# Performance work log

Measured on AMD Instinct MI355X. Metric: run time of the kernel, lower is better.

The kernel has to match this reference:

```python
import jax, jax.numpy as jnp
import numpy as np

N_NODES = 325
C = 64
BATCH = 64
SEQ = 12
K = 3


def setup_inputs() -> dict:
    key = jax.random.key(0)
    k1, k2, k3 = jax.random.split(key, 3)
    x = jax.random.normal(k1, (BATCH, C, N_NODES, SEQ), dtype=jnp.float32)
    # sparse-ish binary adjacency with self loops (typical traffic graph density)
    a = (jax.random.uniform(k2, (N_NODES, N_NODES)) < 0.05).astype(jnp.float32)
    adj = jnp.maximum(a, a.T)
    adj = adj.at[jnp.arange(N_NODES), jnp.arange(N_NODES)].set(1.0)
    W = jax.random.normal(k3, (K, C, C), dtype=jnp.float32) * (1.0 / np.sqrt(C))
    b = jnp.zeros((C,), dtype=jnp.float32)
    return {"x": x, "adj": adj, "W": W, "b": b}


def reference(x, adj, W, b):
    B, c_in, N, T = x.shape
    # [B, C, N, T] -> [B*T, N, C]
    xr = jnp.transpose(x, (0, 3, 2, 1)).reshape(-1, N, c_in)
    # symmetric normalized Laplacian L = I - D^{-1/2} A D^{-1/2}
    d = adj.sum(axis=-1)
    d_inv_sqrt = jnp.where(d > 0, jax.lax.rsqrt(d), 0.0)
    norm_adj = d_inv_sqrt[:, None] * adj * d_inv_sqrt[None, :]
    L = jnp.eye(N, dtype=adj.dtype) - norm_adj
    # Chebyshev recursion, K=3
    Tx0 = xr
    Tx1 = jnp.einsum('ij,bjc->bic', L, Tx0)
    out = jnp.einsum('bnc,cd->bnd', Tx0, W[0]) + jnp.einsum('bnc,cd->bnd', Tx1, W[1])
    Tx2 = 2.0 * jnp.einsum('ij,bjc->bic', L, Tx1) - Tx0
    out = out + jnp.einsum('bnc,cd->bnd', Tx2, W[2]) + b
    # [B*T, N, C] -> [B, C, N, T]
    out = out.reshape(B, T, N, c_in)
    return jnp.transpose(out, (0, 3, 2, 1))
```

## Files before the change

kernel.cpp:

```cpp
#include <hip/hip_runtime.h>
#include <hip/hip_bf16.h>

#define NND   325
#define SEQ   12
#define NT    3900
#define KP    352
#define NC    11
#define CHUNK_SHORTS 12288
#define MROWS 48
#define NTILE 22

typedef __attribute__((ext_vector_type(8))) short short8;
typedef __attribute__((ext_vector_type(4))) float floatx4;

static __device__ __forceinline__ unsigned short f2bf(float f) {
    unsigned int u = __float_as_uint(f);
    unsigned int r = (u + 0x7fffu + ((u >> 16) & 1u)) >> 16;
    return (unsigned short)r;
}

static __device__ __forceinline__ int xi(int m, int j) {
    int slot = (j >> 3) ^ ((m >> 1) & 3);
    return m * KP + slot * 8 + (j & 7);
}
static __device__ __forceinline__ int swz(int n) {
    return ((n & 7) ^ ((n >> 3) & 7)) << 4;
}

__global__ void calc_dis(const float* __restrict__ adj, float* __restrict__ dis) {
    int i = blockIdx.x;
    const float* row = adj + (size_t)i * NND;
    float s = 0.f;
    for (int j = threadIdx.x; j < NND; j += 64) s += row[j];
    for (int o = 32; o; o >>= 1) s += __shfl_down(s, o);
    if (threadIdx.x == 0) dis[i] = (s > 0.f) ? rsqrtf(s) : 0.f;
}

__global__ void build_L2(const float* __restrict__ adj, const float* __restrict__ dis,
                         unsigned short* __restrict__ Lg2) {
    int s = blockIdx.x * 256 + threadIdx.x;
    if (s >= NC * CHUNK_SHORTS) return;
    int c = s / CHUNK_SHORTS, r = s - c * CHUNK_SHORTS;
    int n = r >> 5, w = r & 31;
    int j = c * 32 + w;
    float v = 0.f;
    if (n < NND && j < NND) {
        float a = adj[(size_t)n * NND + j];
        v = ((n == j) ? 1.f : 0.f) - dis[n] * a * dis[j];
    }
    Lg2[s] = f2bf(v);
}

__global__ void build_wswz(const float* __restrict__ W, unsigned short* __restrict__ wswz) {
    int idx = blockIdx.x * 256 + threadIdx.x;
    if (idx >= 64 * 192) return;
    int d = idx / 192, k = idx - d * 192;
    int kind = k >> 6, c = k & 63;
    float wv = W[kind * 4096 + c * 64 + d];
    float w;
    if (kind == 0)      w = wv - W[2 * 4096 + c * 64 + d];
    else if (kind == 1) w = wv;
    else                w = 2.f * wv;
    int byte = d * 384 + ((2 * k) ^ swz(d));
    wswz[byte >> 1] = f2bf(w);
}

__global__ __launch_bounds__(512, 4) void cheb_mfma(
        const float* __restrict__ x,
        const unsigned short* __restrict__ Lg2,
        unsigned short* __restrict__ Yg,
        unsigned short* __restrict__ Zg) {
    __shared__ __align__(16) unsigned short Xs[MROWS * KP];
    __shared__ __align__(16) unsigned short Ys[MROWS * KP];

    const int tid = threadIdx.x;
    int bid = blockIdx.x;
    bid = (bid & 7) * 128 + (bid >> 3);
    const int g0 = bid * 4;

    const int w  = tid >> 6;
    const int l  = tid & 63;
    const int lm = l & 15, lg = l >> 4;
    const int ap = (lm >> 1) & 3;

    const unsigned short* lp[3];
    #pragma unroll
    for (int i = 0; i < 3; ++i) {
        int ti = w * 3 + i;
        int nrow = ti * 16 + lm;
        lp[i] = Lg2 + (size_t)nrow * 32 + lg * 8;
    }
    const int nown = (w * 3 + 2 < NTILE) ? 3 : (NTILE - w * 3 < 0 ? 0 : NTILE - w * 3);

    for (int i = tid; i < MROWS * 27; i += 512) {
        int m = i / 27, j = 325 + (i - (i / 27) * 27);
        Xs[xi(m, j)] = 0;
    }
    const float4* xb = (const float4*)(x + (size_t)g0 * NT);
    for (int i = tid; i < 3900; i += 512) {
        float4 v = xb[i];
        int f = i * 4;
        int gl = f / NT;
        int rem = f - gl * NT;
        int j = rem / SEQ;
        int t0 = rem - j * SEQ;
        int m = gl * SEQ + t0;
        Xs[xi(m + 0, j)] = f2bf(v.x);
        Xs[xi(m + 1, j)] = f2bf(v.y);
        Xs[xi(m + 2, j)] = f2bf(v.z);
        Xs[xi(m + 3, j)] = f2bf(v.w);
    }
    __syncthreads();

    floatx4 acc[3][3];

    auto zero_acc = [&]() {
        #pragma unroll
        for (int a = 0; a < 3; ++a)
            #pragma unroll
            for (int b2 = 0; b2 < 3; ++b2) acc[a][b2] = (floatx4){0.f, 0.f, 0.f, 0.f};
    };

    auto gemm = [&](const unsigned short* Aimg) {
        #pragma unroll
        for (int c = 0; c < NC; ++c) {
            short8 bf[3];
            #pragma unroll
            for (int i = 0; i < 3; ++i)
                if (i < nown)
                    bf[i] = *(const short8*)(lp[i] + (size_t)c * CHUNK_SHORTS);
            short8 af[3];
            #pragma unroll
            for (int mt = 0; mt < 3; ++mt) {
                int m = mt * 16 + lm;
                int slot = (c * 4 + lg) ^ ap;
                af[mt] = *(const short8*)&Aimg[m * KP + slot * 8];
            }
            #pragma unroll
            for (int i = 0; i < 3; ++i)
                if (i < nown)
                    #pragma unroll
                    for (int mt = 0; mt < 3; ++mt)
                        acc[mt][i] = __builtin_amdgcn_mfma_f32_16x16x32_bf16(
                            af[mt], bf[i], acc[mt][i], 0, 0, 0);
        }
    };

    auto store_acc = [&](unsigned short* img) {
        #pragma unroll
        for (int i = 0; i < 3; ++i) {
            if (i < nown) {
                int n = (w * 3 + i) * 16 + lm;
                #pragma unroll
                for (int mt = 0; mt < 3; ++mt)
                    #pragma unroll
                    for (int r = 0; r < 4; ++r)
                        img[xi(mt * 16 + lg * 4 + r, n)] = f2bf(acc[mt][i][r]);
            }
        }
    };

    auto copy_out = [&](const unsigned short* img, unsigned short* dst) {
        for (int i = tid; i < 1950 * 2; i += 512) {
            int gl = i / 975;
            int r2 = i - gl * 975;
            int n = r2 / 3;
            int tq = (r2 - n * 3) * 4;
            int m = gl * SEQ + tq;
            ushort4 u;
            u.x = img[xi(m + 0, n)];
            u.y = img[xi(m + 1, n)];
            u.z = img[xi(m + 2, n)];
            u.w = img[xi(m + 3, n)];
            *(ushort4*)&dst[(size_t)(g0 + gl) * NT + n * SEQ + tq] = u;
        }
    };

    zero_acc();
    gemm(Xs);
    store_acc(Ys);
    __syncthreads();
    copy_out(Ys, Yg);

    zero_acc();
    gemm(Ys);
    store_acc(Xs);
    __syncthreads();
    copy_out(Xs, Zg);
}

__global__ __launch_bounds__(256) void mix_mfma(
        const float* __restrict__ x,
        const unsigned short* __restrict__ Yg,
        const unsigned short* __restrict__ Zg,
        const unsigned short* __restrict__ wswz,
        const float* __restrict__ bias,
        float* __restrict__ out) {
    __shared__ unsigned short Bl[96 * 192];
    __shared__ unsigned short Al[64 * 192];
    const int tid = threadIdx.x;
    int lin = blockIdx.x;
    lin = (lin & 7) * 328 + (lin >> 3);
    const int b = lin / 41;
    const int nt0 = (lin - b * 41) * 96;
    const bool tail = (nt0 + 96 > NT);

    for (int i = tid; i < 1536; i += 256)
        *(short8*)((char*)Al + i * 16) = *(const short8*)((const char*)wswz + i * 16);

    for (int i = tid; i < 768; i += 256) {
        int r = i / 12, ch = i - r * 12;
        int nt = nt0 + ch * 8;
        const float* sp = x + ((size_t)b * 64 + r) * NT + nt;
        float f[8];
        if (!tail || nt + 8 <= NT) {
            float4 v0 = *(const float4*)sp;
            float4 v1 = *(const float4*)(sp + 4);
            f[0] = v0.x; f[1] = v0.y; f[2] = v0.z; f[3] = v0.w;
            f[4] = v1.x; f[5] = v1.y; f[6] = v1.z; f[7] = v1.w;
        } else {
            #pragma unroll
            for (int jj = 0; jj < 8; ++jj) f[jj] = (nt + jj < NT) ? sp[jj] : 0.f;
        }
        int k2 = 2 * r;
        #pragma unroll
        for (int jj = 0; jj < 8; ++jj) {
            int n = ch * 8 + jj;
            *(unsigned short*)((char*)Bl + n * 384 + (k2 ^ swz(n))) = f2bf(f[jj]);
        }
    }
    for (int i = tid; i < 1536; i += 256) {
        int r = 64 + i / 12, ch = i % 12;
        int nt = nt0 + ch * 8;
        const unsigned short* base = (r < 128) ? Yg : Zg;
        const unsigned short* sp = base + ((size_t)b * 64 + (r & 63)) * NT + nt;
        unsigned short f[8];
        if (!tail || nt + 8 <= NT) {
            ushort4 v0 = *(const ushort4*)sp;
            ushort4 v1 = *(const ushort4*)(sp + 4);
            f[0] = v0.x; f[1] = v0.y; f[2] = v0.z; f[3] = v0.w;
            f[4] = v1.x; f[5] = v1.y; f[6] = v1.z; f[7] = v1.w;
        } else {
            #pragma unroll
            for (int jj = 0; jj < 8; ++jj) f[jj] = (nt + jj < NT) ? sp[jj] : (unsigned short)0;
        }
        int k2 = 2 * r;
        #pragma unroll
        for (int jj = 0; jj < 8; ++jj) {
            int n = ch * 8 + jj;
            *(unsigned short*)((char*)Bl + n * 384 + (k2 ^ swz(n))) = f[jj];
        }
    }
    __syncthreads();

    const int w = __builtin_amdgcn_readfirstlane(tid >> 6);
    const int l = tid & 63;
    const int lm = l & 15, lg = l >> 4;

    floatx4 acc[6];
    #pragma unroll
    for (int i = 0; i < 6; ++i) acc[i] = (floatx4){0.f, 0.f, 0.f, 0.f};

    const int arow = w * 16 + lm;
    const char* Ab = (const char*)Al + arow * 384;
    #pragma unroll
    for (int ks = 0; ks < 6; ++ks) {
        const int k2 = (ks * 32 + lg * 8) * 2;
        short8 a = *(const short8*)(Ab + (k2 ^ swz(arow)));
        #pragma unroll
        for (int ni = 0; ni < 6; ++ni) {
            int n = ni * 16 + lm;
            short8 bb = *(const short8*)((const char*)Bl + n * 384 + (k2 ^ swz(n)));
            acc[ni] = __builtin_amdgcn_mfma_f32_16x16x32_bf16(a, bb, acc[ni], 0, 0, 0);
        }
    }

    float br[4];
    #pragma unroll
    for (int j = 0; j < 4; ++j) br[j] = bias[w * 16 + lg * 4 + j];
    #pragma unroll
    for (int ni = 0; ni < 6; ++ni) {
        int nt = nt0 + ni * 16 + lm;
        if (nt < NT) {
            float* op = out + ((size_t)b * 64 + w * 16 + lg * 4) * NT + nt;
            #pragma unroll
            for (int j = 0; j < 4; ++j) op[(size_t)j * NT] = acc[ni][j] + br[j];
        }
    }
}

extern "C" void kernel_launch(void* const* d_in, const int* in_sizes, int n_in,
                              void* d_out, int out_size, void* d_ws, size_t ws_size,
                              hipStream_t stream) {
    const float* x   = (const float*)d_in[0];
    const float* adj = (const float*)d_in[1];
    const float* W   = (const float*)d_in[2];
    const float* b   = (const float*)d_in[3];
    float* out = (float*)d_out;

    char* ws = (char*)d_ws;
    float* dis           = (float*)(ws + 0);
    unsigned short* Lg2  = (unsigned short*)(ws + 1312);
    unsigned short* wswz = (unsigned short*)(ws + 271648);
    unsigned short* Yg   = (unsigned short*)(ws + 296224);
    unsigned short* Zg   = (unsigned short*)(ws + 32245024);

    calc_dis<<<NND, 64, 0, stream>>>(adj, dis);
    build_L2<<<(NC * CHUNK_SHORTS + 255) / 256, 256, 0, stream>>>(adj, dis, Lg2);
    build_wswz<<<48, 256, 0, stream>>>(W, wswz);
    cheb_mfma<<<1024, 512, 0, stream>>>(x, Lg2, Yg, Zg);
    mix_mfma<<<2624, 256, 0, stream>>>(x, Yg, Zg, wswz, b, out);
}
```

Measured before the change: 125.6 us.

## Store Chebyshev intermediates in time-major padded layout with vectorized LDS/global stores

Swaps the MFMA operand roles so each lane's accumulator holds four consecutive nodes for one time row, which allows ushort4 stores into the swizzled LDS image. The global Y/Z intermediates now use a [group][t][node] layout padded to 328 nodes per row, so copy_out moves 16-byte vectors straight from LDS. The mix kernel then gathers a node range per time step with this stride, with no tail handling. This cuts the scalar LDS traffic and the narrow global stores, at the cost of a strided re-gather in the mix kernel and reads of padded node columns.

```diff
diff --git a/kernel.cpp b/kernel.cpp
--- a/kernel.cpp
+++ b/kernel.cpp
@@ -9,6 +9,8 @@
 #define CHUNK_SHORTS 12288
 #define MROWS 48
 #define NTILE 22
+#define TROW  328
+#define GROW  3936
 
 typedef __attribute__((ext_vector_type(8))) short short8;
 typedef __attribute__((ext_vector_type(4))) float floatx4;
@@ -86,8 +88,7 @@
     const unsigned short* lp[3];
     #pragma unroll
     for (int i = 0; i < 3; ++i) {
-        int ti = w * 3 + i;
-        int nrow = ti * 16 + lm;
+        int nrow = (w * 3 + i) * 16 + lm;
         lp[i] = Lg2 + (size_t)nrow * 32 + lg * 8;
     }
     const int nown = (w * 3 + 2 < NTILE) ? 3 : (NTILE - w * 3 < 0 ? 0 : NTILE - w * 3);
@@ -121,28 +122,28 @@
             for (int b2 = 0; b2 < 3; ++b2) acc[a][b2] = (floatx4){0.f, 0.f, 0.f, 0.f};
     };
 
-    auto gemm = [&](const unsigned short* Aimg) {
+    auto gemm = [&](const unsigned short* Bimg) {
         #pragma unroll
         for (int c = 0; c < NC; ++c) {
-            short8 bf[3];
+            short8 lf[3];
             #pragma unroll
             for (int i = 0; i < 3; ++i)
                 if (i < nown)
-                    bf[i] = *(const short8*)(lp[i] + (size_t)c * CHUNK_SHORTS);
-            short8 af[3];
+                    lf[i] = *(const short8*)(lp[i] + (size_t)c * CHUNK_SHORTS);
+            short8 bf[3];
             #pragma unroll
             for (int mt = 0; mt < 3; ++mt) {
                 int m = mt * 16 + lm;
                 int slot = (c * 4 + lg) ^ ap;
-                af[mt] = *(const short8*)&Aimg[m * KP + slot * 8];
+                bf[mt] = *(const short8*)&Bimg[m * KP + slot * 8];
             }
             #pragma unroll
             for (int i = 0; i < 3; ++i)
                 if (i < nown)
                     #pragma unroll
                     for (int mt = 0; mt < 3; ++mt)
-                        acc[mt][i] = __builtin_amdgcn_mfma_f32_16x16x32_bf16(
-                            af[mt], bf[i], acc[mt][i], 0, 0, 0);
+                        acc[i][mt] = __builtin_amdgcn_mfma_f32_16x16x32_bf16(
+                            lf[i], bf[mt], acc[i][mt], 0, 0, 0);
         }
     };
 
@@ -150,29 +151,32 @@
         #pragma unroll
         for (int i = 0; i < 3; ++i) {
             if (i < nown) {
-                int n = (w * 3 + i) * 16 + lm;
+                int n0 = (w * 3 + i) * 16 + lg * 4;
                 #pragma unroll
-                for (int mt = 0; mt < 3; ++mt)
-                    #pragma unroll
-                    for (int r = 0; r < 4; ++r)
-                        img[xi(mt * 16 + lg * 4 + r, n)] = f2bf(acc[mt][i][r]);
+                for (int mt = 0; mt < 3; ++mt) {
+                    int m = mt * 16 + lm;
+                    int slot = (n0 >> 3) ^ ((m >> 1) & 3);
+                    ushort4 u;
+                    u.x = f2bf(acc[i][mt][0]);
+                    u.y = f2bf(acc[i][mt][1]);
+                    u.z = f2bf(acc[i][mt][2]);
+                    u.w = f2bf(acc[i][mt][3]);
+                    *(ushort4*)&img[m * KP + slot * 8 + (n0 & 7)] = u;
+                }
             }
         }
     };
 
     auto copy_out = [&](const unsigned short* img, unsigned short* dst) {
-        for (int i = tid; i < 1950 * 2; i += 512) {
-            int gl = i / 975;
-            int r2 = i - gl * 975;
-            int n = r2 / 3;
-            int tq = (r2 - n * 3) * 4;
-            int m = gl * SEQ + tq;
-            ushort4 u;
-            u.x = img[xi(m + 0, n)];
-            u.y = img[xi(m + 1, n)];
-            u.z = img[xi(m + 2, n)];
-            u.w = img[xi(m + 3, n)];
-            *(ushort4*)&dst[(size_t)(g0 + gl) * NT + n * SEQ + tq] = u;
+        for (int i = tid; i < 4 * SEQ * 41; i += 512) {
+            int gl = i / 492;
+            int r2 = i - gl * 492;
+            int t = r2 / 41;
+            int oct = r2 - t * 41;
+            int m = gl * SEQ + t;
+            int slot = oct ^ ((m >> 1) & 3);
+            short8 v = *(const short8*)&img[m * KP + slot * 8];
+            *(short8*)&dst[(size_t)(g0 + gl) * GROW + t * TROW + oct * 8] = v;
         }
     };
 
@@ -229,26 +233,21 @@
             *(unsigned short*)((char*)Bl + n * 384 + (k2 ^ swz(n))) = f2bf(f[jj]);
         }
     }
+    const int nn0 = nt0 / 12;
     for (int i = tid; i < 1536; i += 256) {
-        int r = 64 + i / 12, ch = i % 12;
-        int nt = nt0 + ch * 8;
+        int r = 64 + i / 12, t = i % 12;
         const unsigned short* base = (r < 128) ? Yg : Zg;
-        const unsigned short* sp = base + ((size_t)b * 64 + (r & 63)) * NT + nt;
+        const unsigned short* sp = base + ((size_t)b * 64 + (r & 63)) * GROW + t * TROW + nn0;
+        ushort4 v0 = *(const ushort4*)sp;
+        ushort4 v1 = *(const ushort4*)(sp + 4);
         unsigned short f[8];
-        if (!tail || nt + 8 <= NT) {
-            ushort4 v0 = *(const ushort4*)sp;
-            ushort4 v1 = *(const ushort4*)(sp + 4);
-            f[0] = v0.x; f[1] = v0.y; f[2] = v0.z; f[3] = v0.w;
-            f[4] = v1.x; f[5] = v1.y; f[6] = v1.z; f[7] = v1.w;
-        } else {
-            #pragma unroll
-            for (int jj = 0; jj < 8; ++jj) f[jj] = (nt + jj < NT) ? sp[jj] : (unsigned short)0;
-        }
+        f[0] = v0.x; f[1] = v0.y; f[2] = v0.z; f[3] = v0.w;
+        f[4] = v1.x; f[5] = v1.y; f[6] = v1.z; f[7] = v1.w;
         int k2 = 2 * r;
         #pragma unroll
         for (int jj = 0; jj < 8; ++jj) {
-            int n = ch * 8 + jj;
-            *(unsigned short*)((char*)Bl + n * 384 + (k2 ^ swz(n))) = f[jj];
+            int q = jj * 12 + t;
+            *(unsigned short*)((char*)Bl + q * 384 + (k2 ^ swz(q))) = f[jj];
         }
     }
     __syncthreads();
@@ -303,7 +302,7 @@
     unsigned short* Lg2  = (unsigned short*)(ws + 1312);
     unsigned short* wswz = (unsigned short*)(ws + 271648);
     unsigned short* Yg   = (unsigned short*)(ws + 296224);
-    unsigned short* Zg   = (unsigned short*)(ws + 32245024);
+    unsigned short* Zg   = (unsigned short*)(ws + 32539936);
 
     calc_dis<<<NND, 64, 0, stream>>>(adj, dis);
     build_L2<<<(NC * CHUNK_SHORTS + 255) / 256, 256, 0, stream>>>(adj, dis, Lg2);
```

New measurement: 126.3 us. About the same (+0.6%).
